# Kernel optimization log

Measured on AMD Instinct MI355X. Metric: run time of the kernel, lower is better.

The kernel has to match this reference:

```python
import jax, jax.numpy as jnp
import numpy as np

H = 512      # hidden_size
NH = 8       # num_attention_heads
HD = H // NH # attention_head_size
B, S = 2, 4096


def setup_inputs() -> dict:
    key = jax.random.key(0)
    ks = jax.random.split(key, 9)
    sc = 1.0 / np.sqrt(H)
    return {
        "hidden_states": jax.random.normal(ks[0], (B, S, H), dtype=jnp.float32),
        "Wq": jax.random.normal(ks[1], (H, H), dtype=jnp.float32) * sc,
        "bq": jnp.zeros((H,), dtype=jnp.float32),
        "Wk": jax.random.normal(ks[2], (H, H), dtype=jnp.float32) * sc,
        "bk": jnp.zeros((H,), dtype=jnp.float32),
        "Wv": jax.random.normal(ks[3], (H, H), dtype=jnp.float32) * sc,
        "bv": jnp.zeros((H,), dtype=jnp.float32),
        "Wo": jax.random.normal(ks[4], (H, H), dtype=jnp.float32) * sc,
        "bo": jnp.zeros((H,), dtype=jnp.float32),
    }


def reference(hidden_states, Wq, bq, Wk, bk, Wv, bv, Wo, bo):
    # QKV projections (nn.Linear: x @ W.T + b)
    def split_heads(x):  # [B,S,H] -> [B,NH,S,HD]
        return x.reshape(B, S, NH, HD).transpose(0, 2, 1, 3)

    q = split_heads(hidden_states @ Wq.T + bq)
    k = split_heads(hidden_states @ Wk.T + bk)
    v = split_heads(hidden_states @ Wv.T + bv)

    scores = jnp.einsum("bhqd,bhkd->bhqk", q, k) / np.sqrt(HD)
    probs = jax.nn.softmax(scores, axis=-1)  # dropout is identity in eval
    ctx = jnp.einsum("bhqk,bhkd->bhqd", probs, v)
    ctx = ctx.transpose(0, 2, 1, 3).reshape(B, S, H)
    return ctx @ Wo.T + bo
```

## Files before the change

kernel.cpp:

```cpp
#include <hip/hip_runtime.h>
#include <hip/hip_bf16.h>
#include <math.h>


typedef __bf16 bf16;
typedef __bf16 bf16x2v __attribute__((ext_vector_type(2)));
typedef __bf16 bf16x4 __attribute__((ext_vector_type(4)));
typedef __bf16 bf16x8 __attribute__((ext_vector_type(8)));
typedef float  f32x4  __attribute__((ext_vector_type(4)));
typedef unsigned int u32x4 __attribute__((ext_vector_type(4)));

#define MFMA16(a, b, c) __builtin_amdgcn_mfma_f32_16x16x32_bf16((a), (b), (c), 0, 0, 0)

__device__ __forceinline__ void gll16(const bf16* g, bf16* l) {
    __builtin_amdgcn_global_load_lds(
        (const __attribute__((address_space(1))) void*)g,
        (__attribute__((address_space(3))) void*)l, 16, 0, 0);
}

__device__ __forceinline__ unsigned int pack2(float lo, float hi) {
    bf16x2v t = {(bf16)lo, (bf16)hi};
    return __builtin_bit_cast(unsigned int, t);
}

__global__ __launch_bounds__(256) void cvt_f32_bf16(const float* __restrict__ src,
                                                    bf16* __restrict__ dst, int n) {
    int i = (blockIdx.x * 256 + threadIdx.x) * 4;
    if (i >= n) return;
    float4 v = *reinterpret_cast<const float4*>(src + i);
    bf16x4 o = {(bf16)v.x, (bf16)v.y, (bf16)v.z, (bf16)v.w};
    *reinterpret_cast<bf16x4*>(dst + i) = o;
}

__global__ __launch_bounds__(256) void cvt_w4(const float* __restrict__ a,
                                              const float* __restrict__ b,
                                              const float* __restrict__ c,
                                              const float* __restrict__ d,
                                              bf16* __restrict__ out) {
    const int y = blockIdx.y;
    const float* src = (y == 0) ? a : (y == 1) ? b : (y == 2) ? c : d;
    int i = (blockIdx.x * 256 + threadIdx.x) * 4;
    float4 v = *reinterpret_cast<const float4*>(src + i);
    bf16x4 o = {(bf16)v.x, (bf16)v.y, (bf16)v.z, (bf16)v.w};
    *reinterpret_cast<bf16x4*>(out + y * 262144 + i) = o;
}

template <int MODE>
__global__ __launch_bounds__(256) void gemm_bt(const bf16* __restrict__ A,
                                               const bf16* __restrict__ W,
                                               const float* __restrict__ b0,
                                               const float* __restrict__ b1,
                                               const float* __restrict__ b2,
                                               bf16* __restrict__ dstbf,
                                               float* __restrict__ dstf) {
    __shared__ bf16 sA[128 * 64];
    __shared__ bf16 sB[128 * 64];

    const int tid = threadIdx.x;
    const int w   = tid >> 6;
    const int l   = tid & 63;
    const int m0  = blockIdx.y * 128;
    const int n0  = blockIdx.x * 128;
    const int z   = blockIdx.z;

    const bf16*  Wz   = (MODE == 0) ? (W + z * 262144) : W;
    const float* bias = (MODE == 0) ? (z == 0 ? b0 : (z == 1 ? b1 : b2)) : b0;
    const float  scale = (MODE == 0 && z == 0) ? 0.125f * 1.4426950408889634f : 1.0f;

    const int wr = (w >> 1) * 64, wc = (w & 1) * 64;
    const int fr = l & 15, fg = l >> 4;

    const int srow0 = tid >> 3;
    const int sgr   = (tid & 7) ^ (srow0 & 7);
    const int ldso  = srow0 * 64 + (tid & 7) * 8;

    f32x4 acc[4][4];
    const f32x4 zero = {0.f, 0.f, 0.f, 0.f};
#pragma unroll
    for (int i = 0; i < 4; i++)
#pragma unroll
        for (int j = 0; j < 4; j++) acc[i][j] = zero;

    for (int kt = 0; kt < 512; kt += 64) {
        __syncthreads();
#pragma unroll
        for (int p = 0; p < 4; p++) {
            const int row = srow0 + 32 * p;
            gll16(A  + (m0 + row) * 512 + kt + sgr * 8, &sA[p * 2048 + ldso]);
            gll16(Wz + (n0 + row) * 512 + kt + sgr * 8, &sB[p * 2048 + ldso]);
        }
        __syncthreads();

#pragma unroll
        for (int ks = 0; ks < 2; ks++) {
            bf16x8 af[4], bfg[4];
#pragma unroll
            for (int mi = 0; mi < 4; mi++)
                af[mi] = *reinterpret_cast<const bf16x8*>(
                    &sA[(wr + mi * 16 + fr) * 64 + (((4 * ks + fg) ^ (fr & 7)) << 3)]);
#pragma unroll
            for (int ni = 0; ni < 4; ni++)
                bfg[ni] = *reinterpret_cast<const bf16x8*>(
                    &sB[(wc + ni * 16 + fr) * 64 + (((4 * ks + fg) ^ (fr & 7)) << 3)]);
#pragma unroll
            for (int mi = 0; mi < 4; mi++)
#pragma unroll
                for (int ni = 0; ni < 4; ni++)
                    acc[mi][ni] = MFMA16(af[mi], bfg[ni], acc[mi][ni]);
        }
    }

#pragma unroll
    for (int mi = 0; mi < 4; mi++) {
#pragma unroll
        for (int ni = 0; ni < 4; ni++) {
            const int gcol = n0 + wc + ni * 16 + fr;
            const float bc = bias[gcol];
#pragma unroll
            for (int r = 0; r < 4; r++) {
                const int grow = m0 + wr + mi * 16 + fg * 4 + r;
                float v = acc[mi][ni][r] + bc;
                if (MODE == 0) {
                    v *= scale;
                    const int bb = grow >> 12, s = grow & 4095;
                    const int hh = gcol >> 6, dd = gcol & 63;
                    size_t idx;
                    if (z == 2) {
                        idx = (size_t)2 * 4194304 +
                              ((size_t)((bb * 8 + hh) * 64 + dd)) * 4096 + s;
                    } else {
                        idx = (size_t)z * 4194304 +
                              ((size_t)((bb * 8 + hh) * 4096 + s) << 6) + dd;
                    }
                    dstbf[idx] = (bf16)v;
                } else {
                    dstf[grow * 512 + gcol] = v;
                }
            }
        }
    }
}

__global__ __launch_bounds__(256, 2) void attn_kernel(const bf16* __restrict__ Q,
                                                      const bf16* __restrict__ K,
                                                      const bf16* __restrict__ Vt,
                                                      bf16* __restrict__ ctx) {
    __shared__ bf16 sKb[2][4096];
    __shared__ bf16 sVb[2][4096];

    const int tid = threadIdx.x;
    const int w   = tid >> 6;
    const int l   = tid & 63;
    const int fr  = l & 15, fg = l >> 4;

    int n = blockIdx.y * 32 + blockIdx.x;
    n = (n & 7) * 64 + (n >> 3);
    const int bh = n >> 5;
    const int q0 = (n & 31) * 128;
    const size_t base = (size_t)bh * 262144;

    const int srow0 = tid >> 3;
    const int sgr   = (tid & 7) ^ (srow0 & 7);
    const int ldso  = srow0 * 64 + (tid & 7) * 8;

    const int ko0 = fr * 64 + (((0 + fg) ^ (fr & 7)) << 3);
    const int ko1 = fr * 64 + (((4 + fg) ^ (fr & 7)) << 3);

#define STAGE(buf, tt)                                                              \
    do {                                                                            \
        _Pragma("unroll")                                                           \
        for (int p = 0; p < 2; p++) {                                               \
            const int row_ = srow0 + 32 * p;                                        \
            gll16(K  + base + (size_t)((tt) + row_) * 64 + sgr * 8,                 \
                  &sKb[buf][p * 2048 + ldso]);                                      \
            gll16(Vt + base + (size_t)row_ * 4096 + (tt) + sgr * 8,                 \
                  &sVb[buf][p * 2048 + ldso]);                                      \
        }                                                                           \
    } while (0)

#define QK_TILE(kb_)                                                                \
    do {                                                                            \
        _Pragma("unroll")                                                           \
        for (int kvb = 0; kvb < 4; kvb++) {                                         \
            const bf16x8 kf0 = *reinterpret_cast<const bf16x8*>((kb_) + ko0 + kvb * 1024); \
            const bf16x8 kf1 = *reinterpret_cast<const bf16x8*>((kb_) + ko1 + kvb * 1024); \
            _Pragma("unroll")                                                       \
            for (int qb = 0; qb < 2; qb++) {                                        \
                sc[kvb][qb] = MFMA16(kf0, qf[0][qb], zero);                         \
                sc[kvb][qb] = MFMA16(kf1, qf[1][qb], sc[kvb][qb]);                  \
            }                                                                       \
        }                                                                           \
    } while (0)

#define PV_TILE()                                                                   \
    do {                                                                            \
        _Pragma("unroll")                                                           \
        for (int ks = 0; ks < 2; ks++) {                                            \
            _Pragma("unroll")                                                       \
            for (int qb = 0; qb < 2; qb++)                                          \
                lacc[qb] = MFMA16(ones, pf[ks][qb], lacc[qb]);                      \
            _Pragma("unroll")                                                       \
            for (int db = 0; db < 4; db++)                                          \
                _Pragma("unroll")                                                   \
                for (int qb = 0; qb < 2; qb++)                                      \
                    o[db][qb] = MFMA16(vf[ks][db], pf[ks][qb], o[db][qb]);          \
        }                                                                           \
    } while (0)

#define VF_READ(vb_)                                                                \
    do {                                                                            \
        _Pragma("unroll")                                                           \
        for (int db = 0; db < 4; db++) {                                            \
            vf[0][db] = *reinterpret_cast<const bf16x8*>((vb_) + ko0 + db * 1024);  \
            vf[1][db] = *reinterpret_cast<const bf16x8*>((vb_) + ko1 + db * 1024);  \
        }                                                                           \
    } while (0)

#define SOFTMAX_PACK()                                                              \
    do {                                                                            \
        _Pragma("unroll")                                                           \
        for (int qb = 0; qb < 2; qb++) {                                            \
            unsigned int c[4][2];                                                   \
            _Pragma("unroll")                                                       \
            for (int kvb = 0; kvb < 4; kvb++) {                                     \
                const float p0 = __builtin_amdgcn_exp2f(sc[kvb][qb][0]);            \
                const float p1 = __builtin_amdgcn_exp2f(sc[kvb][qb][1]);            \
                const float p2 = __builtin_amdgcn_exp2f(sc[kvb][qb][2]);            \
                const float p3 = __builtin_amdgcn_exp2f(sc[kvb][qb][3]);            \
                c[kvb][0] = pack2(p0, p1);                                          \
                c[kvb][1] = pack2(p2, p3);                                          \
            }                                                                       \
            _Pragma("unroll")                                                       \
            for (int ks = 0; ks < 2; ks++) {                                        \
                unsigned int a0 = c[2 * ks][0], b0 = c[2 * ks + 1][0];              \
                unsigned int a1 = c[2 * ks][1], b1 = c[2 * ks + 1][1];              \
                asm("v_permlane32_swap_b32 %0, %1" : "+v"(a0), "+v"(b0));           \
                asm("v_permlane16_swap_b32 %0, %1" : "+v"(a0), "+v"(b0));           \
                asm("v_permlane32_swap_b32 %0, %1" : "+v"(a1), "+v"(b1));           \
                asm("v_permlane16_swap_b32 %0, %1" : "+v"(a1), "+v"(b1));           \
                u32x4 uu = {a0, a1, b0, b1};                                        \
                pf[ks][qb] = __builtin_bit_cast(bf16x8, uu);                        \
            }                                                                       \
        }                                                                           \
    } while (0)

    bf16x8 qf[2][2];
#pragma unroll
    for (int qb = 0; qb < 2; qb++)
#pragma unroll
        for (int ks = 0; ks < 2; ks++)
            qf[ks][qb] = *reinterpret_cast<const bf16x8*>(
                Q + base + (size_t)(q0 + 32 * w + 16 * qb + fr) * 64 + ks * 32 + fg * 8);

    const bf16 one = (bf16)1.0f;
    const bf16x8 ones = {one, one, one, one, one, one, one, one};

    const f32x4 zero = {0.f, 0.f, 0.f, 0.f};
    f32x4 o[4][2];
#pragma unroll
    for (int db = 0; db < 4; db++)
#pragma unroll
        for (int qb = 0; qb < 2; qb++) o[db][qb] = zero;
    f32x4 lacc[2] = {zero, zero};

    f32x4  sc[4][2];
    bf16x8 vf[2][4];
    bf16x8 pf[2][2];

    STAGE(0, 0);
    __syncthreads();
    STAGE(1, 64);
    QK_TILE(sKb[0]);
    VF_READ(sVb[0]);
    SOFTMAX_PACK();

    int pb = 1;
    for (int t = 64; t < 4096; t += 64, pb ^= 1) {
        __syncthreads();
        if (t + 64 < 4096) STAGE(pb ^ 1, t + 64);

        __builtin_amdgcn_s_setprio(1);
        QK_TILE(sKb[pb]);
        PV_TILE();
        __builtin_amdgcn_s_setprio(0);

        VF_READ(sVb[pb]);
        SOFTMAX_PACK();
    }

    __builtin_amdgcn_s_setprio(1);
    PV_TILE();
    __builtin_amdgcn_s_setprio(0);

    const int bb = bh >> 3, hh = bh & 7;
#pragma unroll
    for (int qb = 0; qb < 2; qb++) {
        const float inv = 1.0f / lacc[qb][0];
        const int s = q0 + 32 * w + 16 * qb + fr;
#pragma unroll
        for (int db = 0; db < 4; db++) {
            bf16x4 pr = {(bf16)(o[db][qb][0] * inv), (bf16)(o[db][qb][1] * inv),
                         (bf16)(o[db][qb][2] * inv), (bf16)(o[db][qb][3] * inv)};
            *reinterpret_cast<bf16x4*>(
                &ctx[((size_t)(bb * 4096 + s)) * 512 + hh * 64 + db * 16 + 4 * fg]) = pr;
        }
    }
#undef STAGE
#undef QK_TILE
#undef PV_TILE
#undef VF_READ
#undef SOFTMAX_PACK
}

extern "C" void kernel_launch(void* const* d_in, const int* in_sizes, int n_in,
                              void* d_out, int out_size, void* d_ws, size_t ws_size,
                              hipStream_t stream) {
    const float* X  = (const float*)d_in[0];
    const float* Wq = (const float*)d_in[1];
    const float* bq = (const float*)d_in[2];
    const float* Wk = (const float*)d_in[3];
    const float* bk = (const float*)d_in[4];
    const float* Wv = (const float*)d_in[5];
    const float* bv = (const float*)d_in[6];
    const float* Wo = (const float*)d_in[7];
    const float* bo = (const float*)d_in[8];
    float* out = (float*)d_out;

    bf16* ws  = (bf16*)d_ws;
    bf16* Xbf = ws;
    bf16* Wqb = Xbf + 4194304;
    bf16* Qb  = Wqb + 4 * 262144;
    bf16* Kb  = Qb + 4194304;
    bf16* Vtb = Kb + 4194304;
    bf16* Ctx = Vtb + 4194304;

    cvt_f32_bf16<<<4096, 256, 0, stream>>>(X, Xbf, 4194304);
    cvt_w4<<<dim3(256, 4), 256, 0, stream>>>(Wq, Wk, Wv, Wo, Wqb);

    gemm_bt<0><<<dim3(4, 64, 3), 256, 0, stream>>>(Xbf, Wqb, bq, bk, bv, Qb, nullptr);

    attn_kernel<<<dim3(32, 16), 256, 0, stream>>>(Qb, Kb, Vtb, Ctx);

    gemm_bt<1><<<dim3(4, 64, 1), 256, 0, stream>>>(Ctx, Wqb + 3 * 262144, bo,
                                                   nullptr, nullptr, nullptr, out);
}
```

Measured before the change: 139.6 us.

## Load V fragments directly from global into registers, double-buffered, drop V LDS staging

Removes the shared-memory staging of V^T and instead has each lane load its V MFMA fragments straight from global memory into a register double-buffer (vfA/vfB). The loop is unrolled by two so the two register buffers alternate, and the last tile is handled explicitly. This cuts LDS traffic and footprint, which could allow more overlap. The cost is higher register pressure and global-load latency exposed on the critical path. The float-to-bf16 pair packing is also switched to an inline v_cvt_pk_bf16_f32 instruction.

```diff
diff --git a/kernel.cpp b/kernel.cpp
--- a/kernel.cpp
+++ b/kernel.cpp
@@ -18,9 +18,10 @@
         (__attribute__((address_space(3))) void*)l, 16, 0, 0);
 }
 
-__device__ __forceinline__ unsigned int pack2(float lo, float hi) {
-    bf16x2v t = {(bf16)lo, (bf16)hi};
-    return __builtin_bit_cast(unsigned int, t);
+__device__ __forceinline__ unsigned int cvtpk(float lo, float hi) {
+    unsigned int r;
+    asm("v_cvt_pk_bf16_f32 %0, %1, %2" : "=v"(r) : "v"(lo), "v"(hi));
+    return r;
 }
 
 __global__ __launch_bounds__(256) void cvt_f32_bf16(const float* __restrict__ src,
@@ -146,7 +147,6 @@
                                                       const bf16* __restrict__ Vt,
                                                       bf16* __restrict__ ctx) {
     __shared__ bf16 sKb[2][4096];
-    __shared__ bf16 sVb[2][4096];
 
     const int tid = threadIdx.x;
     const int w   = tid >> 6;
@@ -166,15 +166,28 @@
     const int ko0 = fr * 64 + (((0 + fg) ^ (fr & 7)) << 3);
     const int ko1 = fr * 64 + (((4 + fg) ^ (fr & 7)) << 3);
 
+    const bf16* vtb = Vt + base;
+    int vdo[4];
+#pragma unroll
+    for (int db = 0; db < 4; db++) vdo[db] = (16 * db + fr) * 4096 + 8 * fg;
+
 #define STAGE(buf, tt)                                                              \
     do {                                                                            \
         _Pragma("unroll")                                                           \
         for (int p = 0; p < 2; p++) {                                               \
             const int row_ = srow0 + 32 * p;                                        \
-            gll16(K  + base + (size_t)((tt) + row_) * 64 + sgr * 8,                 \
+            gll16(K + base + (size_t)((tt) + row_) * 64 + sgr * 8,                  \
                   &sKb[buf][p * 2048 + ldso]);                                      \
-            gll16(Vt + base + (size_t)row_ * 4096 + (tt) + sgr * 8,                 \
-                  &sVb[buf][p * 2048 + ldso]);                                      \
+        }                                                                           \
+    } while (0)
+
+#define VF_ISSUE(VBUF, tt)                                                          \
+    do {                                                                            \
+        const bf16* vt_ = vtb + (tt);                                               \
+        _Pragma("unroll")                                                           \
+        for (int db = 0; db < 4; db++) {                                            \
+            VBUF[0][db] = *reinterpret_cast<const bf16x8*>(vt_ + vdo[db]);          \
+            VBUF[1][db] = *reinterpret_cast<const bf16x8*>(vt_ + vdo[db] + 32);     \
         }                                                                           \
     } while (0)
 
@@ -192,7 +205,7 @@
         }                                                                           \
     } while (0)
 
-#define PV_TILE()                                                                   \
+#define PV_TILE(VF)                                                                 \
     do {                                                                            \
         _Pragma("unroll")                                                           \
         for (int ks = 0; ks < 2; ks++) {                                            \
@@ -203,16 +216,7 @@
             for (int db = 0; db < 4; db++)                                          \
                 _Pragma("unroll")                                                   \
                 for (int qb = 0; qb < 2; qb++)                                      \
-                    o[db][qb] = MFMA16(vf[ks][db], pf[ks][qb], o[db][qb]);          \
-        }                                                                           \
-    } while (0)
-
-#define VF_READ(vb_)                                                                \
-    do {                                                                            \
-        _Pragma("unroll")                                                           \
-        for (int db = 0; db < 4; db++) {                                            \
-            vf[0][db] = *reinterpret_cast<const bf16x8*>((vb_) + ko0 + db * 1024);  \
-            vf[1][db] = *reinterpret_cast<const bf16x8*>((vb_) + ko1 + db * 1024);  \
+                    o[db][qb] = MFMA16(VF[ks][db], pf[ks][qb], o[db][qb]);          \
         }                                                                           \
     } while (0)
 
@@ -227,8 +231,8 @@
                 const float p1 = __builtin_amdgcn_exp2f(sc[kvb][qb][1]);            \
                 const float p2 = __builtin_amdgcn_exp2f(sc[kvb][qb][2]);            \
                 const float p3 = __builtin_amdgcn_exp2f(sc[kvb][qb][3]);            \
-                c[kvb][0] = pack2(p0, p1);                                          \
-                c[kvb][1] = pack2(p2, p3);                                          \
+                c[kvb][0] = cvtpk(p0, p1);                                          \
+                c[kvb][1] = cvtpk(p2, p3);                                          \
             }                                                                       \
             _Pragma("unroll")                                                       \
             for (int ks = 0; ks < 2; ks++) {                                        \
@@ -244,6 +248,18 @@
         }                                                                           \
     } while (0)
 
+#define BODY(KBUF, VFOLD, VFNEW, tt)                                                \
+    do {                                                                            \
+        __syncthreads();                                                            \
+        STAGE((KBUF) ^ 1, (tt) + 64);                                               \
+        __builtin_amdgcn_s_setprio(1);                                              \
+        QK_TILE(sKb[KBUF]);                                                         \
+        PV_TILE(VFOLD);                                                             \
+        __builtin_amdgcn_s_setprio(0);                                              \
+        VF_ISSUE(VFNEW, tt);                                                        \
+        SOFTMAX_PACK();                                                             \
+    } while (0)
+
     bf16x8 qf[2][2];
 #pragma unroll
     for (int qb = 0; qb < 2; qb++)
@@ -264,32 +280,31 @@
     f32x4 lacc[2] = {zero, zero};
 
     f32x4  sc[4][2];
-    bf16x8 vf[2][4];
+    bf16x8 vfA[2][4], vfB[2][4];
     bf16x8 pf[2][2];
 
     STAGE(0, 0);
+    VF_ISSUE(vfA, 0);
     __syncthreads();
     STAGE(1, 64);
     QK_TILE(sKb[0]);
-    VF_READ(sVb[0]);
     SOFTMAX_PACK();
 
-    int pb = 1;
-    for (int t = 64; t < 4096; t += 64, pb ^= 1) {
-        __syncthreads();
-        if (t + 64 < 4096) STAGE(pb ^ 1, t + 64);
-
-        __builtin_amdgcn_s_setprio(1);
-        QK_TILE(sKb[pb]);
-        PV_TILE();
-        __builtin_amdgcn_s_setprio(0);
-
-        VF_READ(sVb[pb]);
-        SOFTMAX_PACK();
+    int t = 64;
+    for (int i = 0; i < 31; i++, t += 128) {
+        BODY(1, vfA, vfB, t);
+        BODY(0, vfB, vfA, t + 64);
     }
 
+    __syncthreads();
     __builtin_amdgcn_s_setprio(1);
-    PV_TILE();
+    QK_TILE(sKb[1]);
+    PV_TILE(vfA);
+    __builtin_amdgcn_s_setprio(0);
+    VF_ISSUE(vfB, 4032);
+    SOFTMAX_PACK();
+    __builtin_amdgcn_s_setprio(1);
+    PV_TILE(vfB);
     __builtin_amdgcn_s_setprio(0);
 
     const int bb = bh >> 3, hh = bh & 7;
@@ -306,10 +321,11 @@
         }
     }
 #undef STAGE
+#undef VF_ISSUE
 #undef QK_TILE
 #undef PV_TILE
-#undef VF_READ
 #undef SOFTMAX_PACK
+#undef BODY
 }
 
 extern "C" void kernel_launch(void* const* d_in, const int* in_sizes, int n_in,
```

Result: slower. 186.0 us (+33.2%).
